# Kernel tuning notes

Measured on AMD Instinct MI355X. Metric: run time of the kernel, lower is better.

The kernel has to match this reference:

```python
import jax, jax.numpy as jnp
import numpy as np

N = 100000
E = 1600000
IN_C = 128
HID = 128
NUM_CLASSES = 10


def setup_inputs() -> dict:
    key = jax.random.key(0)
    k1, k2, k3, k4 = jax.random.split(key, 4)
    x = jax.random.normal(k1, (N, IN_C), dtype=jnp.float32)
    edge_index = jax.random.randint(k2, (2, E), 0, N, dtype=jnp.int64)
    # PyG Linear weights are [out, in]; glorot-ish scale
    W1 = jax.random.normal(k3, (HID, IN_C), dtype=jnp.float32) / np.sqrt(IN_C)
    b1 = jnp.zeros((HID,), dtype=jnp.float32)
    W2 = jax.random.normal(k4, (NUM_CLASSES, HID), dtype=jnp.float32) / np.sqrt(HID)
    b2 = jnp.zeros((NUM_CLASSES,), dtype=jnp.float32)
    return {"x": x, "edge_index": edge_index, "W1": W1, "b1": b1, "W2": W2, "b2": b2}


def _gcn_conv(x, W, b, row, col, n):
    """Faithful PyG GCNConv: linear transform, symmetric gcn_norm with self-loops,
    gather-scale-scatter aggregation, then bias."""
    h = x @ W.T  # [N, out]
    # add self loops
    loop = jnp.arange(n, dtype=row.dtype)
    r = jnp.concatenate([row, loop])
    c = jnp.concatenate([col, loop])
    # degree at destination (col), edge weight = 1
    deg = jax.ops.segment_sum(jnp.ones(r.shape[0], dtype=h.dtype), c, num_segments=n)
    dis = jnp.where(deg > 0, jax.lax.rsqrt(deg), 0.0)
    norm = dis[r] * dis[c]  # [E+N]
    msgs = norm[:, None] * h[r]  # gather + scale, [E+N, out]
    out = jax.ops.segment_sum(msgs, c, num_segments=n)  # scatter-add
    return out + b


def reference(x, edge_index, W1, b1, W2, b2):
    row, col = edge_index[0], edge_index[1]
    n = x.shape[0]
    x = _gcn_conv(x, W1, b1, row, col, n)
    x = _gcn_conv(x, W2, b2, row, col, n)
    return x
```

## Files before the change

kernel.cpp:

```cpp
#include <hip/hip_runtime.h>
#include <hip/hip_fp16.h>

#define N_NODES 100000
#define E_EDGES 1600000
#define NCLS 10

#define BW 256
#define NB 391
#define EPB 8192
#define NBLK_BIN 196

__global__ __launch_bounds__(256) void k_hist(const int* __restrict__ col,
                                              int* __restrict__ blockHist) {
    __shared__ int h[NB];
    int t = threadIdx.x;
    for (int i = t; i < NB; i += 256) h[i] = 0;
    __syncthreads();
    int base = blockIdx.x * EPB;
    int end  = min(base + EPB, E_EDGES);
    for (int e = base + t; e < end; e += 256)
        atomicAdd(&h[col[e] >> 8], 1);
    __syncthreads();
    for (int i = t; i < NB; i += 256)
        blockHist[blockIdx.x * NB + i] = h[i];
}

__global__ __launch_bounds__(512) void k_scan_w12(int* __restrict__ blockHist,
                                                  int* __restrict__ bucketBase,
                                                  const float* __restrict__ W1,
                                                  const float* __restrict__ W2,
                                                  const float* __restrict__ b1,
                                                  float* __restrict__ W12,
                                                  float* __restrict__ c1) {
    __shared__ int   s[512];
    __shared__ float w2s[1280];
    int t = threadIdx.x;
    if (blockIdx.x == 0) {
        int run = 0;
        if (t < NB) {
            for (int b = 0; b < NBLK_BIN; ++b) {
                int v = blockHist[b * NB + t];
                blockHist[b * NB + t] = run;
                run += v;
            }
        }
        s[t] = (t < NB) ? run : 0;
        __syncthreads();
        for (int st = 1; st < 512; st <<= 1) {
            int tmp = (t >= st) ? s[t - st] : 0;
            __syncthreads();
            s[t] += tmp;
            __syncthreads();
        }
        if (t < NB) bucketBase[t] = s[t] - run;
        if (t == NB - 1) bucketBase[NB] = s[t];
    } else {
        for (int i = t; i < 1280; i += 512) w2s[i] = W2[i];
        __syncthreads();
        if (t < 128) {
            float acc[NCLS];
            #pragma unroll
            for (int j = 0; j < NCLS; ++j) acc[j] = 0.f;
            for (int m = 0; m < 128; ++m) {
                float w1mk = W1[m * 128 + t];
                #pragma unroll
                for (int j = 0; j < NCLS; ++j) acc[j] += w2s[j * 128 + m] * w1mk;
            }
            #pragma unroll
            for (int j = 0; j < NCLS; ++j) W12[j * 128 + t] = acc[j];
        } else if (t < 144) {
            int j = t - 128;
            float acc = 0.f;
            if (j < NCLS)
                for (int m = 0; m < 128; ++m) acc += W2[j * 128 + m] * b1[m];
            c1[j] = (j < NCLS) ? acc : 0.f;
        }
    }
}

__global__ __launch_bounds__(256) void k_bin(const int* __restrict__ ei,
                                             const int* __restrict__ blockHist,
                                             const int* __restrict__ bucketBase,
                                             unsigned* __restrict__ binned) {
    __shared__ int h[NB];
    __shared__ int chunk[NB];
    int t = threadIdx.x;
    for (int i = t; i < NB; i += 256) {
        h[i] = 0;
        chunk[i] = bucketBase[i] + blockHist[blockIdx.x * NB + i];
    }
    __syncthreads();
    int base = blockIdx.x * EPB;
    int end  = min(base + EPB, E_EDGES);
    const int* col = ei + E_EDGES;
    for (int e = base + t; e < end; e += 256) {
        int c = col[e];
        int r = ei[e];
        int k = c >> 8;
        int slot = chunk[k] + atomicAdd(&h[k], 1);
        binned[slot] = ((unsigned)r << 8) | (unsigned)(c & 255);
    }
}

__global__ __launch_bounds__(256) void k_build(const unsigned* __restrict__ binned,
                                               const int* __restrict__ bucketBase,
                                               int2* __restrict__ od,
                                               float* __restrict__ dis,
                                               int* __restrict__ csr,
                                               const float* __restrict__ x,
                                               const float* __restrict__ W12,
                                               __half2* __restrict__ g1h) {
    __shared__ int cnt[BW];
    __shared__ int sc[BW];
    __shared__ int eoff[BW];
    __shared__ int cur[BW];
    int k = blockIdx.x;
    int t = threadIdx.x;
    cnt[t] = 0;
    __syncthreads();
    int s0 = bucketBase[k], s1 = bucketBase[k + 1];
    for (int i = s0 + t; i < s1; i += 256)
        atomicAdd(&cnt[binned[i] & 255], 1);
    __syncthreads();
    int v = cnt[t];
    sc[t] = v;
    __syncthreads();
    for (int st = 1; st < 256; st <<= 1) {
        int tmp = (t >= st) ? sc[t - st] : 0;
        __syncthreads();
        sc[t] += tmp;
        __syncthreads();
    }
    eoff[t] = sc[t] - v;
    cur[t] = 0;
    int node = k * BW + t;
    float d = rsqrtf((float)(v + 1));
    if (node < N_NODES) {
        od[node] = make_int2(s0 + eoff[t], v);
        dis[node] = d;
    }
    __syncthreads();
    for (int i = s0 + t; i < s1; i += 256) {
        unsigned p = binned[i];
        int lc = p & 255;
        int r  = p >> 8;
        int pos = s0 + eoff[lc] + atomicAdd(&cur[lc], 1);
        csr[pos] = r;
    }

    if (node < N_NODES) {
        const float4* x4 = (const float4*)x;
        float acc[NCLS];
        #pragma unroll
        for (int j = 0; j < NCLS; ++j) acc[j] = 0.f;

        #pragma unroll
        for (int k4 = 0; k4 < 32; ++k4) {
            float4 xv = x4[node * 32 + k4];
            #pragma unroll
            for (int j = 0; j < NCLS; ++j) {
                const float* wj = &W12[j * 128 + k4 * 4];
                acc[j] += xv.x * wj[0] + xv.y * wj[1] + xv.z * wj[2] + xv.w * wj[3];
            }
        }

        __half2 hp[8];
        #pragma unroll
        for (int j = 0; j < 5; ++j)
            hp[j] = __floats2half2_rn(d * acc[2 * j], d * acc[2 * j + 1]);
        hp[5] = __floats2half2_rn(0.f, 0.f);
        hp[6] = hp[5];
        hp[7] = hp[5];
        uint4* dst = (uint4*)&g1h[node * 8];
        dst[0] = *(const uint4*)&hp[0];
        dst[1] = *(const uint4*)&hp[4];
    }
}

__global__ __launch_bounds__(256) void k_agg_a(const __half2* __restrict__ g1h,
                                               const float* __restrict__ dis,
                                               const int* __restrict__ csr,
                                               const int2* __restrict__ od,
                                               const float* __restrict__ c1,
                                               __half2* __restrict__ h2h) {
    int c = blockIdx.x * 32 + (threadIdx.x >> 3);
    int j = threadIdx.x & 7;
    if (c >= N_NODES) return;

    float2 acc = __half22float2(g1h[c * 8 + j]);

    int2 odv  = od[c];
    int start = odv.x;
    int deg   = odv.y;
    int k = 0;
    if (deg >= 4) {
        int i0 = csr[start + 0], i1 = csr[start + 1];
        int i2 = csr[start + 2], i3 = csr[start + 3];
        for (; k + 8 <= deg; k += 4) {
            int n0 = csr[start + k + 4], n1 = csr[start + k + 5];
            int n2 = csr[start + k + 6], n3 = csr[start + k + 7];
            float2 a0 = __half22float2(g1h[i0 * 8 + j]);
            float2 a1 = __half22float2(g1h[i1 * 8 + j]);
            float2 a2 = __half22float2(g1h[i2 * 8 + j]);
            float2 a3 = __half22float2(g1h[i3 * 8 + j]);
            acc.x += (a0.x + a1.x) + (a2.x + a3.x);
            acc.y += (a0.y + a1.y) + (a2.y + a3.y);
            i0 = n0; i1 = n1; i2 = n2; i3 = n3;
        }
        float2 a0 = __half22float2(g1h[i0 * 8 + j]);
        float2 a1 = __half22float2(g1h[i1 * 8 + j]);
        float2 a2 = __half22float2(g1h[i2 * 8 + j]);
        float2 a3 = __half22float2(g1h[i3 * 8 + j]);
        acc.x += (a0.x + a1.x) + (a2.x + a3.x);
        acc.y += (a0.y + a1.y) + (a2.y + a3.y);
        k += 4;
    }
    for (; k < deg; ++k) {
        float2 a = __half22float2(g1h[csr[start + k] * 8 + j]);
        acc.x += a.x;
        acc.y += a.y;
    }

    float dc = dis[c];
    float ox = dc * (dc * acc.x + c1[2 * j]);
    float oy = dc * (dc * acc.y + c1[2 * j + 1]);
    h2h[c * 8 + j] = __floats2half2_rn(ox, oy);
}

__global__ __launch_bounds__(256) void k_agg_b(const __half2* __restrict__ h2h,
                                               const float* __restrict__ dis,
                                               const int* __restrict__ csr,
                                               const int2* __restrict__ od,
                                               const float* __restrict__ b2,
                                               float* __restrict__ out) {
    int c = blockIdx.x * 32 + (threadIdx.x >> 3);
    int j = threadIdx.x & 7;
    if (c >= N_NODES) return;

    float2 acc = __half22float2(h2h[c * 8 + j]);

    int2 odv  = od[c];
    int start = odv.x;
    int deg   = odv.y;
    int k = 0;
    if (deg >= 4) {
        int i0 = csr[start + 0], i1 = csr[start + 1];
        int i2 = csr[start + 2], i3 = csr[start + 3];
        for (; k + 8 <= deg; k += 4) {
            int n0 = csr[start + k + 4], n1 = csr[start + k + 5];
            int n2 = csr[start + k + 6], n3 = csr[start + k + 7];
            float2 a0 = __half22float2(h2h[i0 * 8 + j]);
            float2 a1 = __half22float2(h2h[i1 * 8 + j]);
            float2 a2 = __half22float2(h2h[i2 * 8 + j]);
            float2 a3 = __half22float2(h2h[i3 * 8 + j]);
            acc.x += (a0.x + a1.x) + (a2.x + a3.x);
            acc.y += (a0.y + a1.y) + (a2.y + a3.y);
            i0 = n0; i1 = n1; i2 = n2; i3 = n3;
        }
        float2 a0 = __half22float2(h2h[i0 * 8 + j]);
        float2 a1 = __half22float2(h2h[i1 * 8 + j]);
        float2 a2 = __half22float2(h2h[i2 * 8 + j]);
        float2 a3 = __half22float2(h2h[i3 * 8 + j]);
        acc.x += (a0.x + a1.x) + (a2.x + a3.x);
        acc.y += (a0.y + a1.y) + (a2.y + a3.y);
        k += 4;
    }
    for (; k < deg; ++k) {
        float2 a = __half22float2(h2h[csr[start + k] * 8 + j]);
        acc.x += a.x;
        acc.y += a.y;
    }

    if (j < 5) {
        float dc = dis[c];
        float2 o;
        o.x = dc * acc.x + b2[2 * j];
        o.y = dc * acc.y + b2[2 * j + 1];
        *(float2*)&out[c * NCLS + 2 * j] = o;
    }
}

extern "C" void kernel_launch(void* const* d_in, const int* in_sizes, int n_in,
                              void* d_out, int out_size, void* d_ws, size_t ws_size,
                              hipStream_t stream) {
    const float* x  = (const float*)d_in[0];
    const int*   ei = (const int*)d_in[1];
    const float* W1 = (const float*)d_in[2];
    const float* b1 = (const float*)d_in[3];
    const float* W2 = (const float*)d_in[4];
    const float* b2 = (const float*)d_in[5];
    float* out = (float*)d_out;

    char* ws = (char*)d_ws;
    int*      bucketBase = (int*)(ws + 0);
    float*    W12        = (float*)(ws + 4096);
    float*    c1         = (float*)(ws + 16384);
    int*      blockHist  = (int*)(ws + 32768);
    int2*     od         = (int2*)(ws + (1 << 20));
    float*    dis        = (float*)(ws + (3 << 20));
    unsigned* binned     = (unsigned*)(ws + (4 << 20));
    int*      csr        = (int*)(ws + (12 << 20));
    __half2*  g1h        = (__half2*)(ws + (20 << 20));
    __half2*  h2h        = (__half2*)(ws + (24 << 20));

    k_hist<<<NBLK_BIN, 256, 0, stream>>>(ei + E_EDGES, blockHist);
    k_scan_w12<<<2, 512, 0, stream>>>(blockHist, bucketBase, W1, W2, b1, W12, c1);
    k_bin<<<NBLK_BIN, 256, 0, stream>>>(ei, blockHist, bucketBase, binned);
    k_build<<<NB, 256, 0, stream>>>(binned, bucketBase, od, dis, csr, x, W12, g1h);

    k_agg_a<<<(N_NODES + 31) / 32, 256, 0, stream>>>(g1h, dis, csr, od, c1, h2h);
    k_agg_b<<<(N_NODES + 31) / 32, 256, 0, stream>>>(h2h, dis, csr, od, b2, out);
}
```

Baseline: 105.9 us.

## Move x·W12 projection into scan kernel and fold W12 build into histogram

The W12/c1 weight-folding work now rides as an extra block in the histogram kernel, and the 128->10 projection of x moves from k_build into the scan kernel's spare blocks, writing unscaled fp32 results to a workspace buffer. k_build then only reads these precomputed values, scales them by the degree norm and packs them to half. The aim is to fill the otherwise nearly idle scan launch with useful work and shorten the critical path through k_build. The cost is an extra fp32 intermediate write and read of about 6.4 MB, plus more workspace.

```diff
diff --git a/kernel.cpp b/kernel.cpp
--- a/kernel.cpp
+++ b/kernel.cpp
@@ -10,52 +10,28 @@
 #define EPB 8192
 #define NBLK_BIN 196
 
-__global__ __launch_bounds__(256) void k_hist(const int* __restrict__ col,
-                                              int* __restrict__ blockHist) {
-    __shared__ int h[NB];
-    int t = threadIdx.x;
-    for (int i = t; i < NB; i += 256) h[i] = 0;
-    __syncthreads();
-    int base = blockIdx.x * EPB;
-    int end  = min(base + EPB, E_EDGES);
-    for (int e = base + t; e < end; e += 256)
-        atomicAdd(&h[col[e] >> 8], 1);
-    __syncthreads();
-    for (int i = t; i < NB; i += 256)
-        blockHist[blockIdx.x * NB + i] = h[i];
-}
-
-__global__ __launch_bounds__(512) void k_scan_w12(int* __restrict__ blockHist,
-                                                  int* __restrict__ bucketBase,
+__global__ __launch_bounds__(256) void k_hist_w12(const int* __restrict__ col,
+                                                  int* __restrict__ blockHist,
                                                   const float* __restrict__ W1,
                                                   const float* __restrict__ W2,
                                                   const float* __restrict__ b1,
                                                   float* __restrict__ W12,
                                                   float* __restrict__ c1) {
-    __shared__ int   s[512];
+    __shared__ int   h[NB];
     __shared__ float w2s[1280];
     int t = threadIdx.x;
-    if (blockIdx.x == 0) {
-        int run = 0;
-        if (t < NB) {
-            for (int b = 0; b < NBLK_BIN; ++b) {
-                int v = blockHist[b * NB + t];
-                blockHist[b * NB + t] = run;
-                run += v;
-            }
-        }
-        s[t] = (t < NB) ? run : 0;
-        __syncthreads();
-        for (int st = 1; st < 512; st <<= 1) {
-            int tmp = (t >= st) ? s[t - st] : 0;
-            __syncthreads();
-            s[t] += tmp;
-            __syncthreads();
-        }
-        if (t < NB) bucketBase[t] = s[t] - run;
-        if (t == NB - 1) bucketBase[NB] = s[t];
+    if (blockIdx.x < NBLK_BIN) {
+        for (int i = t; i < NB; i += 256) h[i] = 0;
+        __syncthreads();
+        int base = blockIdx.x * EPB;
+        int end  = min(base + EPB, E_EDGES);
+        for (int e = base + t; e < end; e += 256)
+            atomicAdd(&h[col[e] >> 8], 1);
+        __syncthreads();
+        for (int i = t; i < NB; i += 256)
+            blockHist[blockIdx.x * NB + i] = h[i];
     } else {
-        for (int i = t; i < 1280; i += 512) w2s[i] = W2[i];
+        for (int i = t; i < 1280; i += 256) w2s[i] = W2[i];
         __syncthreads();
         if (t < 128) {
             float acc[NCLS];
@@ -78,6 +54,58 @@
     }
 }
 
+__global__ __launch_bounds__(512) void k_scan_g1(int* __restrict__ blockHist,
+                                                 int* __restrict__ bucketBase,
+                                                 const float* __restrict__ x,
+                                                 const float* __restrict__ W12,
+                                                 float* __restrict__ g1u) {
+    __shared__ int s[512];
+    int t = threadIdx.x;
+    if (blockIdx.x == 0) {
+        int run = 0;
+        if (t < NB) {
+            for (int b = 0; b < NBLK_BIN; ++b) {
+                int v = blockHist[b * NB + t];
+                blockHist[b * NB + t] = run;
+                run += v;
+            }
+        }
+        s[t] = (t < NB) ? run : 0;
+        __syncthreads();
+        for (int st = 1; st < 512; st <<= 1) {
+            int tmp = (t >= st) ? s[t - st] : 0;
+            __syncthreads();
+            s[t] += tmp;
+            __syncthreads();
+        }
+        if (t < NB) bucketBase[t] = s[t] - run;
+        if (t == NB - 1) bucketBase[NB] = s[t];
+    } else {
+        int row = (blockIdx.x - 1) * 512 + t;
+        if (row >= N_NODES) return;
+
+        const float4* x4 = (const float4*)x;
+        float acc[NCLS];
+        #pragma unroll
+        for (int j = 0; j < NCLS; ++j) acc[j] = 0.f;
+
+        #pragma unroll
+        for (int k4 = 0; k4 < 32; ++k4) {
+            float4 xv = x4[row * 32 + k4];
+            #pragma unroll
+            for (int j = 0; j < NCLS; ++j) {
+                const float* wj = &W12[j * 128 + k4 * 4];
+                acc[j] += xv.x * wj[0] + xv.y * wj[1] + xv.z * wj[2] + xv.w * wj[3];
+            }
+        }
+
+        float4* dst = (float4*)&g1u[row * 16];
+        dst[0] = make_float4(acc[0], acc[1], acc[2], acc[3]);
+        dst[1] = make_float4(acc[4], acc[5], acc[6], acc[7]);
+        dst[2] = make_float4(acc[8], acc[9], 0.f, 0.f);
+    }
+}
+
 __global__ __launch_bounds__(256) void k_bin(const int* __restrict__ ei,
                                              const int* __restrict__ blockHist,
                                              const int* __restrict__ bucketBase,
@@ -107,8 +135,7 @@
                                                int2* __restrict__ od,
                                                float* __restrict__ dis,
                                                int* __restrict__ csr,
-                                               const float* __restrict__ x,
-                                               const float* __restrict__ W12,
+                                               const float* __restrict__ g1u,
                                                __half2* __restrict__ g1h) {
     __shared__ int cnt[BW];
     __shared__ int sc[BW];
@@ -138,6 +165,23 @@
     if (node < N_NODES) {
         od[node] = make_int2(s0 + eoff[t], v);
         dis[node] = d;
+
+        const float4* g4 = (const float4*)&g1u[node * 16];
+        float4 a = g4[0];
+        float4 b = g4[1];
+        float4 c = g4[2];
+        __half2 hp[8];
+        hp[0] = __floats2half2_rn(d * a.x, d * a.y);
+        hp[1] = __floats2half2_rn(d * a.z, d * a.w);
+        hp[2] = __floats2half2_rn(d * b.x, d * b.y);
+        hp[3] = __floats2half2_rn(d * b.z, d * b.w);
+        hp[4] = __floats2half2_rn(d * c.x, d * c.y);
+        hp[5] = __floats2half2_rn(0.f, 0.f);
+        hp[6] = hp[5];
+        hp[7] = hp[5];
+        uint4* dst = (uint4*)&g1h[node * 8];
+        dst[0] = *(const uint4*)&hp[0];
+        dst[1] = *(const uint4*)&hp[4];
     }
     __syncthreads();
     for (int i = s0 + t; i < s1; i += 256) {
@@ -146,34 +190,6 @@
         int r  = p >> 8;
         int pos = s0 + eoff[lc] + atomicAdd(&cur[lc], 1);
         csr[pos] = r;
-    }
-
-    if (node < N_NODES) {
-        const float4* x4 = (const float4*)x;
-        float acc[NCLS];
-        #pragma unroll
-        for (int j = 0; j < NCLS; ++j) acc[j] = 0.f;
-
-        #pragma unroll
-        for (int k4 = 0; k4 < 32; ++k4) {
-            float4 xv = x4[node * 32 + k4];
-            #pragma unroll
-            for (int j = 0; j < NCLS; ++j) {
-                const float* wj = &W12[j * 128 + k4 * 4];
-                acc[j] += xv.x * wj[0] + xv.y * wj[1] + xv.z * wj[2] + xv.w * wj[3];
-            }
-        }
-
-        __half2 hp[8];
-        #pragma unroll
-        for (int j = 0; j < 5; ++j)
-            hp[j] = __floats2half2_rn(d * acc[2 * j], d * acc[2 * j + 1]);
-        hp[5] = __floats2half2_rn(0.f, 0.f);
-        hp[6] = hp[5];
-        hp[7] = hp[5];
-        uint4* dst = (uint4*)&g1h[node * 8];
-        dst[0] = *(const uint4*)&hp[0];
-        dst[1] = *(const uint4*)&hp[4];
     }
 }
 
@@ -300,13 +316,15 @@
     float*    dis        = (float*)(ws + (3 << 20));
     unsigned* binned     = (unsigned*)(ws + (4 << 20));
     int*      csr        = (int*)(ws + (12 << 20));
-    __half2*  g1h        = (__half2*)(ws + (20 << 20));
-    __half2*  h2h        = (__half2*)(ws + (24 << 20));
-
-    k_hist<<<NBLK_BIN, 256, 0, stream>>>(ei + E_EDGES, blockHist);
-    k_scan_w12<<<2, 512, 0, stream>>>(blockHist, bucketBase, W1, W2, b1, W12, c1);
+    float*    g1u        = (float*)(ws + (20 << 20));
+    __half2*  g1h        = (__half2*)(ws + (28 << 20));
+    __half2*  h2h        = (__half2*)(ws + (32 << 20));
+
+    k_hist_w12<<<NBLK_BIN + 1, 256, 0, stream>>>(ei + E_EDGES, blockHist,
+                                                 W1, W2, b1, W12, c1);
+    k_scan_g1<<<NBLK_BIN + 1, 512, 0, stream>>>(blockHist, bucketBase, x, W12, g1u);
     k_bin<<<NBLK_BIN, 256, 0, stream>>>(ei, blockHist, bucketBase, binned);
-    k_build<<<NB, 256, 0, stream>>>(binned, bucketBase, od, dis, csr, x, W12, g1h);
+    k_build<<<NB, 256, 0, stream>>>(binned, bucketBase, od, dis, csr, g1u, g1h);
 
     k_agg_a<<<(N_NODES + 31) / 32, 256, 0, stream>>>(g1h, dis, csr, od, c1, h2h);
     k_agg_b<<<(N_NODES + 31) / 32, 256, 0, stream>>>(h2h, dis, csr, od, b2, out);
```

Result: no change. 104.0 us (-1.8%).
